# Kernel tuning notes

Measured on AMD Instinct MI355X. Metric: run time of the kernel, lower is better.

Reference implementation:

```python
import jax, jax.numpy as jnp
import numpy as np
from jax import lax

DIM = 64        # Branch(dim)
OUT = 2048      # TimesBlock out_channels == TTT model_dim
NH = 8          # num_heads
HD = OUT // NH  # 256 head dim
INNER = 4 * HD  # ttt_mlp hidden
MB = 10         # mini_batch_size
BASE_LR = 0.1   # ttt_base_lr
NK = 6          # TimesBlock num_kernels (k = 1,3,5,7,9,11)
LN_EPS = 1e-6


def _gelu(x):
    return jax.nn.gelu(x, approximate=False)


def _gelu_bwd(x):
    return 0.5 * (1.0 + lax.erf(x / jnp.sqrt(2.0))) + x * jnp.exp(-0.5 * x * x) / jnp.sqrt(2.0 * jnp.pi)


def _ttt_head(qs, ks, vs, W1h, b1h, W2h, b2h, gw, gb):
    # qs/ks/vs: [NC, MB, HD]; sequential scan over mini-batch chunks (TTT inner GD)
    eta = BASE_LR / MB

    def step(carry, chunk):
        W1c, b1c, W2c, b2c = carry
        xq, xk, xv = chunk
        Z1 = xk @ W1c + b1c              # [MB, INNER]
        A1 = _gelu(Z1)
        Z2 = A1 @ W2c + b2c              # [MB, HD]
        # grad of 0.5*||LN(Z2) - (xv - xk)||^2 wrt Z2 (fused LN l2 backward)
        tgt = xv - xk
        mu = Z2.mean(-1, keepdims=True)
        std = jnp.sqrt(Z2.var(-1, keepdims=True) + LN_EPS)
        xhat = (2 * 0 + Z2 - mu) / std
        gout = (gw * xhat + gb) - tgt
        gxh = gout * gw
        gZ2 = (gxh - gxh.mean(-1, keepdims=True) - xhat * (gxh * xhat).mean(-1, keepdims=True)) / std
        gZ1 = (gZ2 @ W2c.T) * _gelu_bwd(Z1)
        # inner-model SGD step
        W1n = W1c - eta * (xk.T @ gZ1)
        b1n = b1c - eta * gZ1.sum(0)
        W2n = W2c - eta * (A1.T @ gZ2)
        b2n = b2c - eta * gZ2.sum(0)
        # apply updated inner model to queries, post-LN + residual
        Z1q = xq @ W1n + b1n
        Z2q = _gelu(Z1q) @ W2n + b2n
        muq = Z2q.mean(-1, keepdims=True)
        stdq = jnp.sqrt(Z2q.var(-1, keepdims=True) + LN_EPS)
        out = xq + gw * ((Z2q - muq) / stdq) + gb
        return (W1n, b1n, W2n, b2n), out

    _, outs = lax.scan(step, (W1h, b1h, W2h, b2h), (qs, ks, vs))
    return outs.reshape(-1, HD)  # [T, HD]


def _forward(x, seg, conv_ws, conv_bs, wq, wk, wv, wo, W1, b1, W2, b2, ln_w, ln_b):
    B, T, C = x.shape
    xg = jnp.transpose(x, (0, 2, 1)).reshape(B, C, T // seg, seg)
    dn = ('NCHW', 'OIHW', 'NCHW')
    acc = 0.0
    for w, bc in zip(conv_ws, conv_bs):
        acc = acc + lax.conv_general_dilated(xg, w, (1, 1), 'SAME', dimension_numbers=dn) + bc[None, :, None, None]
    xb = acc / float(len(conv_ws))            # TimesBlock: mean over kernel ensemble
    xb = jax.nn.silu(xb)
    xb = jnp.transpose(xb.reshape(B, OUT, T), (0, 2, 1))  # [B, T, OUT]

    def heads(h):  # [B,T,OUT] -> [B,NH,NC,MB,HD]
        return jnp.transpose(h.reshape(B, T, NH, HD), (0, 2, 1, 3)).reshape(B, NH, T // MB, MB, HD)

    q = heads(xb @ wq.T)
    k = heads(xb @ wk.T)
    v = heads(xb @ wv.T)
    f = jax.vmap(jax.vmap(_ttt_head, in_axes=(0, 0, 0, 0, 0, 0, 0, 0, 0)),
                 in_axes=(0, 0, 0, None, None, None, None, None, None))
    o = f(q, k, v, W1, b1, W2, b2, ln_w, ln_b)  # [B, NH, T, HD]
    o = jnp.transpose(o, (0, 2, 1, 3)).reshape(B, T, OUT)
    return o @ wo.T


def setup_inputs() -> dict:
    key = jax.random.key(0)
    ks = jax.random.split(key, 24)
    B, T = 2, 400
    inp = {"x": jax.random.normal(ks[0], (B, T, DIM), jnp.float32), "seg": 20}
    for i in range(NK):
        kk = 2 * i + 1
        fan_out = OUT * kk * kk
        inp[f"conv_w{i}"] = jax.random.normal(ks[1 + i], (OUT, DIM, kk, kk), jnp.float32) * np.sqrt(2.0 / fan_out)
        inp[f"conv_b{i}"] = jnp.zeros((OUT,), jnp.float32)
    for j, nm in enumerate(["wq", "wk", "wv", "wo"]):
        inp[nm] = jax.random.normal(ks[8 + j], (OUT, OUT), jnp.float32) * 0.02
    inp["W1"] = jax.random.normal(ks[12], (NH, HD, INNER), jnp.float32) * 0.02
    inp["b1"] = jnp.zeros((NH, INNER), jnp.float32)
    inp["W2"] = jax.random.normal(ks[13], (NH, INNER, HD), jnp.float32) * 0.02
    inp["b2"] = jnp.zeros((NH, HD), jnp.float32)
    inp["ln_w"] = jnp.ones((NH, HD), jnp.float32)
    inp["ln_b"] = jnp.zeros((NH, HD), jnp.float32)
    return inp


def reference(x, seg, conv_w0, conv_b0, conv_w1, conv_b1, conv_w2, conv_b2,
              conv_w3, conv_b3, conv_w4, conv_b4, conv_w5, conv_b5,
              wq, wk, wv, wo, W1, b1, W2, b2, ln_w, ln_b):
    conv_ws = [conv_w0, conv_w1, conv_w2, conv_w3, conv_w4, conv_w5]
    conv_bs = [conv_b0, conv_b1, conv_b2, conv_b3, conv_b4, conv_b5]
    return _forward(x, seg, conv_ws, conv_bs, wq, wk, wv, wo, W1, b1, W2, b2, ln_w, ln_b)
```

## Files before the change

kernel.cpp:

```cpp
#include <hip/hip_runtime.h>


typedef __bf16 bf16x8 __attribute__((ext_vector_type(8)));
typedef float  f32x4  __attribute__((ext_vector_type(4)));

__device__ __forceinline__ unsigned short f2bf(float f){
  unsigned int u = __builtin_bit_cast(unsigned int, f);
  u += 0x7fffu + ((u >> 16) & 1u);
  return (unsigned short)(u >> 16);
}
__device__ __forceinline__ float bf2f(unsigned short b){
  unsigned int u = ((unsigned int)b) << 16;
  return __builtin_bit_cast(float, u);
}
__device__ __forceinline__ float gelu_f(float x){
  return 0.5f * x * (1.0f + erff(x * 0.70710678118654752f));
}
__device__ __forceinline__ float gelu_bwd_f(float x){
  return 0.5f * (1.0f + erff(x * 0.70710678118654752f))
       + x * __expf(-0.5f * x * x) * 0.3989422804014327f;
}

__device__ __forceinline__ float2 aload2(const float* p){
  unsigned long long v = __hip_atomic_load((const unsigned long long*)p,
                                           __ATOMIC_RELAXED, __HIP_MEMORY_SCOPE_AGENT);
  union { unsigned long long u; float2 f; } cv; cv.u = v; return cv.f;
}
__device__ __forceinline__ void aadd(float* p, float v){
  __hip_atomic_fetch_add(p, v, __ATOMIC_RELAXED, __HIP_MEMORY_SCOPE_AGENT);
}


__global__ __launch_bounds__(256) void k_weff(
    const float* __restrict__ w0, const float* __restrict__ w1,
    const float* __restrict__ w2, const float* __restrict__ w3,
    const float* __restrict__ w4, const float* __restrict__ w5,
    const float* __restrict__ b0, const float* __restrict__ b1,
    const float* __restrict__ b2, const float* __restrict__ b3,
    const float* __restrict__ b4, const float* __restrict__ b5,
    unsigned short* __restrict__ weff, float* __restrict__ bsum)
{
  extern __shared__ float sw[];
  const int off[6] = {0, 64, 640, 2240, 5376, 10560};
  const float* ws6[6] = {w0, w1, w2, w3, w4, w5};
  int o = blockIdx.x, tid = threadIdx.x;
  if (tid == 0)
    bsum[o] = b0[o] + b1[o] + b2[o] + b3[o] + b4[o] + b5[o];
#pragma unroll
  for (int i = 0; i < 6; i++){
    int kk = 2 * i + 1, sz = 64 * kk * kk;
    const float* src = ws6[i] + (size_t)o * sz;
    for (int idx = tid; idx < sz; idx += 256) sw[off[i] + idx] = src[idx];
  }
  __syncthreads();
  for (int t = tid; t < 7744; t += 256){
    int c = t / 121, dd = t % 121, di = dd / 11, dj = dd % 11;
    float s = 0.f;
#pragma unroll
    for (int i = 0; i < 6; i++){
      int kk = 2 * i + 1;
      int a = di - 5 + i, b = dj - 5 + i;
      if (a >= 0 && a < kk && b >= 0 && b < kk)
        s += sw[off[i] + (c * kk + a) * kk + b];
    }
    weff[(size_t)o * 7744 + t] = f2bf(s);
  }
}

__global__ __launch_bounds__(256) void k_im2col(
    const float* __restrict__ x, unsigned short* __restrict__ P)
{
  int idx = blockIdx.x * 256 + threadIdx.x;
  if (idx >= 800 * 7744) return;
  int n = idx / 7744, k = idx % 7744;
  int c = k / 121, dd = k % 121, di = dd / 11, dj = dd % 11;
  int b = n / 400, pos = n % 400, i = pos / 20, j = pos % 20;
  int ii = i + di - 5, jj = j + dj - 5;
  float v = 0.f;
  if (ii >= 0 && ii < 20 && jj >= 0 && jj < 20)
    v = x[((size_t)b * 400 + ii * 20 + jj) * 64 + c];
  P[idx] = f2bf(v);
}

__global__ __launch_bounds__(256) void k_wqkv(
    const float* __restrict__ wq, const float* __restrict__ wk,
    const float* __restrict__ wv, unsigned short* __restrict__ dst)
{
  int idx = blockIdx.x * 256 + threadIdx.x;
  if (idx >= 6144 * 2048) return;
  int m = idx >> 11, kk = idx & 2047;
  const float* src = (m < 2048) ? wq : ((m < 4096) ? wk : wv);
  dst[idx] = f2bf(src[(size_t)(m & 2047) * 2048 + kk]);
}

__global__ __launch_bounds__(256) void k_f2bf_copy(
    const float* __restrict__ src, unsigned short* __restrict__ dst, int n)
{
  int idx = blockIdx.x * 256 + threadIdx.x;
  if (idx < n) dst[idx] = f2bf(src[idx]);
}

__global__ __launch_bounds__(256) void k_comb_silu(
    const float* __restrict__ p0, const float* __restrict__ p1,
    const float* __restrict__ bsum, unsigned short* __restrict__ xb)
{
  int i4 = (blockIdx.x * 256 + threadIdx.x) * 4;
  float4 a = *(const float4*)&p0[i4];
  float4 b = *(const float4*)&p1[i4];
  int mm = i4 & 2047;
  float4 bs = *(const float4*)&bsum[mm];
  float v[4] = {a.x + b.x + bs.x, a.y + b.y + bs.y, a.z + b.z + bs.z, a.w + b.w + bs.w};
  ushort4 o;
#pragma unroll
  for (int i = 0; i < 4; i++){
    float t = v[i] * (1.0f / 6.0f);
    float sv = t / (1.0f + __expf(-t));
    ((unsigned short*)&o)[i] = f2bf(sv);
  }
  *(ushort4*)&xb[i4] = o;
}

__global__ __launch_bounds__(256) void k_comb_add4(
    const float* __restrict__ p, float* __restrict__ out)
{
  int i4 = (blockIdx.x * 256 + threadIdx.x) * 4;
  float4 a = *(const float4*)&p[i4];
  float4 b = *(const float4*)&p[1638400 + i4];
  float4 c = *(const float4*)&p[3276800 + i4];
  float4 d = *(const float4*)&p[4915200 + i4];
  float4 o = {a.x + b.x + c.x + d.x, a.y + b.y + c.y + d.y,
              a.z + b.z + c.z + d.z, a.w + b.w + c.w + d.w};
  *(float4*)&out[i4] = o;
}

template<int MODE>
__global__ __launch_bounds__(256, 1) void k_gemm(
    const unsigned short* __restrict__ A, const unsigned short* __restrict__ B,
    int M, int N, int lda, int ldb, int kLen,
    unsigned short* __restrict__ qb, unsigned short* __restrict__ kb,
    unsigned short* __restrict__ vb, float* __restrict__ outf)
{
  __shared__ unsigned short As[128 * 32];
  __shared__ unsigned short Bs[128 * 32];
  int tid = threadIdx.x, w = tid >> 6, l = tid & 63, qd = l >> 4, lm = l & 15;
  int m0 = blockIdx.x * 128, n0 = blockIdx.y * 128;
  int kBase = blockIdx.z * kLen;

  f32x4 acc[4][4];
#pragma unroll
  for (int i = 0; i < 4; i++)
#pragma unroll
    for (int j = 0; j < 4; j++){ acc[i][j][0]=0.f; acc[i][j][1]=0.f; acc[i][j][2]=0.f; acc[i][j][3]=0.f; }

  int nk = kLen >> 5;
  for (int kt = 0; kt < nk; kt++){
    int k0 = kBase + (kt << 5);
#pragma unroll
    for (int i = 0; i < 2; i++){
      int cidx = tid + i * 256;
      int row = cidx >> 2, kc = (cidx & 3) << 3;
      *(uint4*)&As[row * 32 + kc] = *(const uint4*)&A[(size_t)(m0 + row) * lda + k0 + kc];
      int br = n0 + row; if (br >= N) br = N - 1;
      *(uint4*)&Bs[row * 32 + kc] = *(const uint4*)&B[(size_t)br * ldb + k0 + kc];
    }
    __syncthreads();
    bf16x8 af[4], bfv[4];
#pragma unroll
    for (int i = 0; i < 4; i++)
      af[i] = *(const bf16x8*)&As[((w >> 1) * 64 + i * 16 + lm) * 32 + qd * 8];
#pragma unroll
    for (int j = 0; j < 4; j++)
      bfv[j] = *(const bf16x8*)&Bs[((w & 1) * 64 + j * 16 + lm) * 32 + qd * 8];
#pragma unroll
    for (int i = 0; i < 4; i++)
#pragma unroll
      for (int j = 0; j < 4; j++)
        acc[i][j] = __builtin_amdgcn_mfma_f32_16x16x32_bf16(af[i], bfv[j], acc[i][j], 0, 0, 0);
    __syncthreads();
  }

#pragma unroll
  for (int i = 0; i < 4; i++){
    int mBase = m0 + (w >> 1) * 64 + i * 16 + qd * 4;
#pragma unroll
    for (int j = 0; j < 4; j++){
      int n = n0 + (w & 1) * 64 + j * 16 + lm;
      if (n < N){
#pragma unroll
        for (int rr = 0; rr < 4; rr++){
          float val = acc[i][j][rr];
          int mm = mBase + rr;
          if (MODE == 1){
            int proj = mm >> 11, o = mm & 2047, hh = o >> 8, d = o & 255;
            int bh = (n / 400) * 8 + hh, tt = n % 400;
            unsigned short* dst = (proj == 0) ? qb : ((proj == 1) ? kb : vb);
            dst[((size_t)bh * 400 + tt) * 256 + d] = f2bf(val);
          } else {
            outf[(size_t)blockIdx.z * M * N + (size_t)n * M + mm] = val;
          }
        }
      }
    }
  }
}

#define O_W1BT 0
#define O_W2K  16896
#define O_W2N  33792
#define O_XKQ  52224
#define O_TGT  54864
#define O_A1   57424
#define O_A1T  58144
#define O_GZ2  60192
#define O_GZ1  62832
#define O_XQ2  64880
#define O_GZ2T 67520
#define O_XKT  73664
#define O_A1Q  79808
#define O_F32  80528
#define O_GW   81168
#define O_GB   81424
#define US_TOTAL 81680
#define TTT_LDS_BYTES (81680 * 2)

#define A1T_IDX(r, c) (O_A1T + ((((r) * 32) + (c)) ^ (((r) & 3) << 3)))
#define GZ1_IDX(r, c) (O_GZ1 + ((((r) * 32) + (c)) ^ (((r) & 3) << 3)))

#define ETA 0.01f
#define BAR_STRIDE 32

__global__ __launch_bounds__(256, 1) void k_ttt(
    const unsigned short* __restrict__ qg, const unsigned short* __restrict__ kg,
    const unsigned short* __restrict__ vg,
    const float* __restrict__ W1g, const float* __restrict__ b1g,
    const float* __restrict__ W2g, const float* __restrict__ b2g,
    const float* __restrict__ gwg, const float* __restrict__ gbg,
    float* __restrict__ z2acc, unsigned short* __restrict__ zqp,
    unsigned int* __restrict__ bar)
{
  extern __shared__ unsigned short lds[];
  float* ldsf = (float*)&lds[O_F32];

  int tid = threadIdx.x, w = tid >> 6, l = tid & 63, qd = l >> 4, lm = l & 15;
  int bid = blockIdx.x;
  int jj = bid >> 3, xx = bid & 7;
  int h  = xx + 8 * (jj >> 4);
  int sl = jj & 15;
  int hh = h & 7;

  for (int i = tid; i < US_TOTAL; i += 256) lds[i] = 0;
  __syncthreads();

  float w1r[4][4][4];
#pragma unroll
  for (int a = 0; a < 4; a++)
#pragma unroll
    for (int nt = 0; nt < 4; nt++)
#pragma unroll
      for (int rr = 0; rr < 4; rr++)
        w1r[a][nt][rr] = W1g[((size_t)hh * 256 + (4 * w + a) * 16 + qd * 4 + rr) * 1024
                             + sl * 64 + nt * 16 + lm];
  float w2r[16][4];
#pragma unroll
  for (int nt = 0; nt < 16; nt++)
#pragma unroll
    for (int rr = 0; rr < 4; rr++)
      w2r[nt][rr] = W2g[((size_t)hh * 1024 + sl * 64 + w * 16 + qd * 4 + rr) * 256
                        + nt * 16 + lm];
  if (tid < 64)  ldsf[tid] = b1g[hh * 1024 + sl * 64 + tid];
  if (tid < 256){
    ldsf[64 + tid] = b2g[hh * 256 + tid];
    lds[O_GW + tid] = f2bf(gwg[hh * 256 + tid]);
    lds[O_GB + tid] = f2bf(gbg[hh * 256 + tid]);
  }

#define WRITE_W1BF() do { \
  _Pragma("unroll") for (int a = 0; a < 4; a++){ \
    int m0i = (4 * w + a) * 16 + qd * 4; \
    _Pragma("unroll") for (int nt = 0; nt < 4; nt++){ \
      int n = nt * 16 + lm; \
      unsigned int p0 = f2bf(w1r[a][nt][0]) | ((unsigned int)f2bf(w1r[a][nt][1]) << 16); \
      unsigned int p1 = f2bf(w1r[a][nt][2]) | ((unsigned int)f2bf(w1r[a][nt][3]) << 16); \
      *(unsigned int*)&lds[O_W1BT + n * 264 + m0i]     = p0; \
      *(unsigned int*)&lds[O_W1BT + n * 264 + m0i + 2] = p1; \
    } } } while(0)

#define WRITE_W2BF() do { \
  int mB = w * 16 + qd * 4; \
  _Pragma("unroll") for (int nt = 0; nt < 16; nt++){ \
    int n = nt * 16 + lm; \
    _Pragma("unroll") for (int rr = 0; rr < 4; rr++) \
      lds[O_W2K + (mB + rr) * 264 + n] = f2bf(w2r[nt][rr]); \
    unsigned int p0 = f2bf(w2r[nt][0]) | ((unsigned int)f2bf(w2r[nt][1]) << 16); \
    unsigned int p1 = f2bf(w2r[nt][2]) | ((unsigned int)f2bf(w2r[nt][3]) << 16); \
    *(unsigned int*)&lds[O_W2N + n * 72 + mB]     = p0; \
    *(unsigned int*)&lds[O_W2N + n * 72 + mB + 2] = p1; \
  } } while(0)

  const size_t hb2 = (size_t)h * 400 * 256;

  unsigned int kreg[5], vreg[5];

#define LOAD_XK_REGS(NCH) do { \
  const unsigned int* kp = (const unsigned int*)(kg + hb2 + (size_t)(NCH) * 2560); \
  const unsigned int* vp = (const unsigned int*)(vg + hb2 + (size_t)(NCH) * 2560); \
  _Pragma("unroll") for (int i5 = 0; i5 < 5; i5++){ \
    kreg[i5] = kp[i5 * 256 + tid]; \
    vreg[i5] = vp[i5 * 256 + tid]; \
  } } while(0)

#define COMMIT_XK_TGT() do { \
  _Pragma("unroll") for (int i5 = 0; i5 < 5; i5++){ \
    int f2i = i5 * 256 + tid; \
    unsigned int ku = kreg[i5], vu = vreg[i5]; \
    int row = f2i >> 7, col = (f2i & 127) * 2; \
    *(unsigned int*)&lds[O_XKQ + row * 264 + col] = ku; \
    lds[O_XKT + col * 24 + row]       = (unsigned short)(ku & 0xffffu); \
    lds[O_XKT + (col + 1) * 24 + row] = (unsigned short)(ku >> 16); \
    float kv0 = bf2f((unsigned short)(ku & 0xffffu)), kv1 = bf2f((unsigned short)(ku >> 16)); \
    float vv0 = bf2f((unsigned short)(vu & 0xffffu)), vv1 = bf2f((unsigned short)(vu >> 16)); \
    unsigned int tu = (unsigned int)f2bf(vv0 - kv0) | ((unsigned int)f2bf(vv1 - kv1) << 16); \
    *(unsigned int*)&lds[O_TGT + row * 256 + col] = tu; \
  } } while(0)

#define LOAD_XQ(NCH) do { \
  const unsigned int* qp = (const unsigned int*)(qg + hb2 + (size_t)(NCH) * 2560); \
  _Pragma("unroll") for (int i5 = 0; i5 < 5; i5++){ \
    int f2i = i5 * 256 + tid; \
    unsigned int qu = qp[f2i]; \
    int row = f2i >> 7, col = (f2i & 127) * 2; \
    *(unsigned int*)&lds[O_XQ2 + row * 264 + col] = qu; \
  } } while(0)

  WRITE_W1BF();
  WRITE_W2BF();
  LOAD_XK_REGS(0);
  COMMIT_XK_TGT();
  LOAD_XQ(0);
  __syncthreads();

  for (int nch = 0; nch < 40; nch++){
    const size_t chunkBase = (size_t)(h * 40 + nch) * 10 * 256;

    bf16x8 w1f[8];
#pragma unroll
    for (int ks = 0; ks < 8; ks++)
      w1f[ks] = *(const bf16x8*)&lds[O_W1BT + (w * 16 + lm) * 264 + ks * 32 + qd * 8];
    float b1n = ldsf[w * 16 + lm];

    f32x4 z1a; z1a[0]=0.f; z1a[1]=0.f; z1a[2]=0.f; z1a[3]=0.f;
#pragma unroll
    for (int ks = 0; ks < 8; ks++){
      bf16x8 av = *(const bf16x8*)&lds[O_XKQ + lm * 264 + ks * 32 + qd * 8];
      z1a = __builtin_amdgcn_mfma_f32_16x16x32_bf16(av, w1f[ks], z1a, 0, 0, 0);
    }
    float z1v[4];
#pragma unroll
    for (int rr = 0; rr < 4; rr++){
      z1v[rr] = z1a[rr] + b1n;
      int mr = qd * 4 + rr;
      if (mr < 10){
        float a1 = gelu_f(z1v[rr]);
        unsigned short ab = f2bf(a1);
        lds[O_A1 + mr * 72 + w * 16 + lm] = ab;
        lds[A1T_IDX(w * 16 + lm, mr)] = ab;
      }
    }
    __syncthreads();

    bf16x8 a1f[2], w2f[4][2];
#pragma unroll
    for (int ks = 0; ks < 2; ks++)
      a1f[ks] = *(const bf16x8*)&lds[O_A1 + lm * 72 + ks * 32 + qd * 8];
#pragma unroll
    for (int nt4 = 0; nt4 < 4; nt4++)
#pragma unroll
      for (int ks = 0; ks < 2; ks++)
        w2f[nt4][ks] = *(const bf16x8*)&lds[O_W2N + ((4 * w + nt4) * 16 + lm) * 72 + ks * 32 + qd * 8];

#pragma unroll
    for (int nt4 = 0; nt4 < 4; nt4++){
      int nt = 4 * w + nt4;
      f32x4 p; p[0]=0.f; p[1]=0.f; p[2]=0.f; p[3]=0.f;
#pragma unroll
      for (int ks = 0; ks < 2; ks++)
        p = __builtin_amdgcn_mfma_f32_16x16x32_bf16(a1f[ks], w2f[nt4][ks], p, 0, 0, 0);
#pragma unroll
      for (int rr = 0; rr < 4; rr++){
        int mr = qd * 4 + rr;
        if (mr < 10)
          aadd(&z2acc[chunkBase + (size_t)mr * 256 + nt * 16 + lm], p[rr]);
      }
    }
    __syncthreads();

    if (tid == 0)
      __hip_atomic_fetch_add(bar + h * BAR_STRIDE, 1u, __ATOMIC_RELAXED, __HIP_MEMORY_SCOPE_AGENT);

    if (nch + 1 < 40)
      LOAD_XK_REGS(nch + 1);

    if (nch > 0){
      f32x4 zq; zq[0]=0.f; zq[1]=0.f; zq[2]=0.f; zq[3]=0.f;
#pragma unroll
      for (int ks = 0; ks < 8; ks++){
        bf16x8 av = *(const bf16x8*)&lds[O_XQ2 + lm * 264 + ks * 32 + qd * 8];
        zq = __builtin_amdgcn_mfma_f32_16x16x32_bf16(av, w1f[ks], zq, 0, 0, 0);
      }
#pragma unroll
      for (int rr = 0; rr < 4; rr++){
        int mr = qd * 4 + rr;
        if (mr < 10)
          lds[O_A1Q + mr * 72 + w * 16 + lm] = f2bf(gelu_f(zq[rr] + b1n));
      }
    }
    __syncthreads();

    if (nch > 0){
      LOAD_XQ(nch);
      unsigned short* zq_out = zqp + ((size_t)(h * 16 + sl) * 40 + (nch - 1)) * 2560;
      bf16x8 a1qf[2];
#pragma unroll
      for (int ks = 0; ks < 2; ks++)
        a1qf[ks] = *(const bf16x8*)&lds[O_A1Q + lm * 72 + ks * 32 + qd * 8];
#pragma unroll
      for (int nt4 = 0; nt4 < 4; nt4++){
        int nt = 4 * w + nt4;
        f32x4 p; p[0]=0.f; p[1]=0.f; p[2]=0.f; p[3]=0.f;
#pragma unroll
        for (int ks = 0; ks < 2; ks++)
          p = __builtin_amdgcn_mfma_f32_16x16x32_bf16(a1qf[ks], w2f[nt4][ks], p, 0, 0, 0);
        float bb = (sl == 0) ? ldsf[64 + nt * 16 + lm] : 0.f;
#pragma unroll
        for (int rr = 0; rr < 4; rr++){
          int mr = qd * 4 + rr;
          if (mr < 10)
            zq_out[mr * 256 + nt * 16 + lm] = f2bf(p[rr] + bb);
        }
      }
    }

    if (tid == 0){
      unsigned int target = 16u * (unsigned int)(nch + 1);
      unsigned int spins = 0;
      while (__hip_atomic_load(bar + h * BAR_STRIDE, __ATOMIC_RELAXED, __HIP_MEMORY_SCOPE_AGENT) < target
             && spins < 8000000u){ spins++; __builtin_amdgcn_s_sleep(1); }
    }
    __syncthreads();

    for (int r2 = w; r2 < 10; r2 += 4){
      int c0 = l * 4;
      const float* bp = &z2acc[chunkBase + (size_t)r2 * 256 + c0];
      float2 u01 = aload2(bp);
      float2 u23 = aload2(bp + 2);
      float zz[4] = {u01.x, u01.y, u23.x, u23.y};
      float s1 = 0.f, s2 = 0.f;
#pragma unroll
      for (int i = 0; i < 4; i++){ zz[i] += ldsf[64 + c0 + i]; s1 += zz[i]; s2 += zz[i] * zz[i]; }
#pragma unroll
      for (int off = 32; off >= 1; off >>= 1){ s1 += __shfl_xor(s1, off, 64); s2 += __shfl_xor(s2, off, 64); }
      float mu = s1 * (1.f / 256.f);
      float var = s2 * (1.f / 256.f) - mu * mu;
      float rstd = rsqrtf(var + 1e-6f);
      float xh[4], gx[4];
      float t1 = 0.f, t2 = 0.f;
#pragma unroll
      for (int i = 0; i < 4; i++){
        xh[i] = (zz[i] - mu) * rstd;
        float gwv = bf2f(lds[O_GW + c0 + i]), gbv = bf2f(lds[O_GB + c0 + i]);
        float tg = bf2f(lds[O_TGT + r2 * 256 + c0 + i]);
        float go = gwv * xh[i] + gbv - tg;
        gx[i] = go * gwv;
        t1 += gx[i]; t2 += gx[i] * xh[i];
      }
#pragma unroll
      for (int off = 32; off >= 1; off >>= 1){ t1 += __shfl_xor(t1, off, 64); t2 += __shfl_xor(t2, off, 64); }
      float m1 = t1 * (1.f / 256.f), m2 = t2 * (1.f / 256.f);
      float g0 = (gx[0] - m1 - xh[0] * m2) * rstd;
      float g1 = (gx[1] - m1 - xh[1] * m2) * rstd;
      float g2 = (gx[2] - m1 - xh[2] * m2) * rstd;
      float g3 = (gx[3] - m1 - xh[3] * m2) * rstd;
      unsigned int p0 = f2bf(g0) | ((unsigned int)f2bf(g1) << 16);
      unsigned int p1 = f2bf(g2) | ((unsigned int)f2bf(g3) << 16);
      *(unsigned int*)&lds[O_GZ2 + r2 * 264 + c0]     = p0;
      *(unsigned int*)&lds[O_GZ2 + r2 * 264 + c0 + 2] = p1;
    }
    __syncthreads();

    {
      float sum = 0.f;
#pragma unroll
      for (int r2 = 0; r2 < 10; r2++){
        unsigned short g = lds[O_GZ2 + r2 * 264 + tid];
        lds[O_GZ2T + tid * 24 + r2] = g;
        sum += bf2f(g);
      }
      ldsf[64 + tid] -= ETA * sum;
    }
    {
      f32x4 g1a; g1a[0]=0.f; g1a[1]=0.f; g1a[2]=0.f; g1a[3]=0.f;
#pragma unroll
      for (int ks = 0; ks < 8; ks++){
        bf16x8 av = *(const bf16x8*)&lds[O_GZ2 + lm * 264 + ks * 32 + qd * 8];
        bf16x8 bv = *(const bf16x8*)&lds[O_W2K + (w * 16 + lm) * 264 + ks * 32 + qd * 8];
        g1a = __builtin_amdgcn_mfma_f32_16x16x32_bf16(av, bv, g1a, 0, 0, 0);
      }
#pragma unroll
      for (int rr = 0; rr < 4; rr++){
        int mr = qd * 4 + rr;
        if (mr < 10){
          float gz1 = g1a[rr] * gelu_bwd_f(z1v[rr]);
          lds[GZ1_IDX(w * 16 + lm, mr)] = f2bf(gz1);
        }
      }
    }
    __syncthreads();

    if (tid < 64){
      float sum = 0.f;
#pragma unroll
      for (int kx = 0; kx < 10; kx++) sum += bf2f(lds[GZ1_IDX(tid, kx)]);
      ldsf[tid] -= ETA * sum;
    }
#pragma unroll
    for (int a = 0; a < 4; a++){
      int mt = 4 * w + a;
      bf16x8 av = *(const bf16x8*)&lds[O_XKT + (mt * 16 + lm) * 24 + (qd & 1) * 8];
#pragma unroll
      for (int nt = 0; nt < 4; nt++){
        bf16x8 bv = *(const bf16x8*)&lds[GZ1_IDX(nt * 16 + lm, qd * 8)];
        f32x4 d; d[0]=0.f; d[1]=0.f; d[2]=0.f; d[3]=0.f;
        d = __builtin_amdgcn_mfma_f32_16x16x32_bf16(av, bv, d, 0, 0, 0);
#pragma unroll
        for (int rr = 0; rr < 4; rr++) w1r[a][nt][rr] -= ETA * d[rr];
      }
    }
    {
      bf16x8 av2 = *(const bf16x8*)&lds[A1T_IDX(w * 16 + lm, qd * 8)];
#pragma unroll
      for (int nt = 0; nt < 16; nt++){
        bf16x8 bv = *(const bf16x8*)&lds[O_GZ2T + (nt * 16 + lm) * 24 + (qd & 1) * 8];
        f32x4 d; d[0]=0.f; d[1]=0.f; d[2]=0.f; d[3]=0.f;
        d = __builtin_amdgcn_mfma_f32_16x16x32_bf16(av2, bv, d, 0, 0, 0);
#pragma unroll
        for (int rr = 0; rr < 4; rr++) w2r[nt][rr] -= ETA * d[rr];
      }
    }
    WRITE_W1BF();
    WRITE_W2BF();
    __syncthreads();

    if (nch + 1 < 40){
      COMMIT_XK_TGT();
    }
    __syncthreads();
  }

  {
    f32x4 zq; zq[0]=0.f; zq[1]=0.f; zq[2]=0.f; zq[3]=0.f;
#pragma unroll
    for (int ks = 0; ks < 8; ks++){
      bf16x8 av = *(const bf16x8*)&lds[O_XQ2 + lm * 264 + ks * 32 + qd * 8];
      bf16x8 bv = *(const bf16x8*)&lds[O_W1BT + (w * 16 + lm) * 264 + ks * 32 + qd * 8];
      zq = __builtin_amdgcn_mfma_f32_16x16x32_bf16(av, bv, zq, 0, 0, 0);
    }
    float b1n = ldsf[w * 16 + lm];
#pragma unroll
    for (int rr = 0; rr < 4; rr++){
      int mr = qd * 4 + rr;
      if (mr < 10)
        lds[O_A1Q + mr * 72 + w * 16 + lm] = f2bf(gelu_f(zq[rr] + b1n));
    }
  }
  __syncthreads();
  {
    unsigned short* zq_out = zqp + ((size_t)(h * 16 + sl) * 40 + 39) * 2560;
#pragma unroll
    for (int nt4 = 0; nt4 < 4; nt4++){
      int nt = 4 * w + nt4;
      f32x4 p; p[0]=0.f; p[1]=0.f; p[2]=0.f; p[3]=0.f;
#pragma unroll
      for (int ks = 0; ks < 2; ks++){
        bf16x8 av = *(const bf16x8*)&lds[O_A1Q + lm * 72 + ks * 32 + qd * 8];
        bf16x8 bv = *(const bf16x8*)&lds[O_W2N + (nt * 16 + lm) * 72 + ks * 32 + qd * 8];
        p = __builtin_amdgcn_mfma_f32_16x16x32_bf16(av, bv, p, 0, 0, 0);
      }
      float bb = (sl == 0) ? ldsf[64 + nt * 16 + lm] : 0.f;
#pragma unroll
      for (int rr = 0; rr < 4; rr++){
        int mr = qd * 4 + rr;
        if (mr < 10)
          zq_out[mr * 256 + nt * 16 + lm] = f2bf(p[rr] + bb);
      }
    }
  }
}

__global__ __launch_bounds__(256) void k_lnout(
    const unsigned short* __restrict__ zqp, const unsigned short* __restrict__ qg,
    const float* __restrict__ gwg, const float* __restrict__ gbg,
    unsigned short* __restrict__ obf)
{
  int w = threadIdx.x >> 6, l = threadIdx.x & 63;
  int gr = blockIdx.x * 4 + w;
  int h = gr / 400, t = gr % 400, hh = h & 7, b = h >> 3;
  int nch = t / 10, mr = t % 10;
  int c0 = l * 4;
  float z[4] = {0.f, 0.f, 0.f, 0.f};
#pragma unroll
  for (int sl = 0; sl < 16; sl++){
    const unsigned short* zp = zqp + (((size_t)(h * 16 + sl) * 40 + nch) * 10 + mr) * 256 + c0;
    ushort4 u = *(const ushort4*)zp;
    z[0] += bf2f(u.x); z[1] += bf2f(u.y); z[2] += bf2f(u.z); z[3] += bf2f(u.w);
  }
  float s1 = 0.f, s2 = 0.f;
#pragma unroll
  for (int i = 0; i < 4; i++){ s1 += z[i]; s2 += z[i] * z[i]; }
#pragma unroll
  for (int off = 32; off >= 1; off >>= 1){ s1 += __shfl_xor(s1, off, 64); s2 += __shfl_xor(s2, off, 64); }
  float mu = s1 * (1.f / 256.f);
  float var = s2 * (1.f / 256.f) - mu * mu;
  float rstd = rsqrtf(var + 1e-6f);
  const unsigned short* qp = &qg[((size_t)h * 400 + t) * 256];
  ushort4 qu = *(const ushort4*)&qp[c0];
  float qv[4] = {bf2f(qu.x), bf2f(qu.y), bf2f(qu.z), bf2f(qu.w)};
  unsigned short* op = &obf[((size_t)(b * 400 + t)) * 2048 + hh * 256];
#pragma unroll
  for (int i = 0; i < 4; i++){
    float xh = (z[i] - mu) * rstd;
    float o = qv[i] + gwg[hh * 256 + c0 + i] * xh + gbg[hh * 256 + c0 + i];
    op[c0 + i] = f2bf(o);
  }
}

#define WS_WEFF   0u
#define WS_P      31719424u
#define WS_WQKV   44109824u
#define WS_WOB    52428800u
#define WS_Z2ACC  62722048u
#define WS_XB     69275648u
#define WS_Q      72552448u
#define WS_K      75829248u
#define WS_V      79106048u
#define WS_OBF    82382848u
#define WS_BSUM   85659648u
#define WS_BAR    85667840u

extern "C" void kernel_launch(void* const* d_in, const int* in_sizes, int n_in,
                              void* d_out, int out_size, void* d_ws, size_t ws_size,
                              hipStream_t stream)
{
  (void)in_sizes; (void)n_in; (void)out_size; (void)ws_size;
  const float* x  = (const float*)d_in[0];
  const float* cw[6]; const float* cb[6];
  for (int i = 0; i < 6; i++){ cw[i] = (const float*)d_in[2 + 2 * i]; cb[i] = (const float*)d_in[3 + 2 * i]; }
  const float* wq  = (const float*)d_in[14];
  const float* wk  = (const float*)d_in[15];
  const float* wv  = (const float*)d_in[16];
  const float* wo  = (const float*)d_in[17];
  const float* W1  = (const float*)d_in[18];
  const float* b1  = (const float*)d_in[19];
  const float* W2  = (const float*)d_in[20];
  const float* b2  = (const float*)d_in[21];
  const float* lnw = (const float*)d_in[22];
  const float* lnb = (const float*)d_in[23];
  float* outf = (float*)d_out;

  char* wsb = (char*)d_ws;
  unsigned short* weff = (unsigned short*)(wsb + WS_WEFF);
  unsigned short* P    = (unsigned short*)(wsb + WS_P);
  unsigned short* wqkv = (unsigned short*)(wsb + WS_WQKV);
  unsigned short* wob  = (unsigned short*)(wsb + WS_WOB);
  unsigned short* xb   = (unsigned short*)(wsb + WS_XB);
  unsigned short* qb   = (unsigned short*)(wsb + WS_Q);
  unsigned short* kb   = (unsigned short*)(wsb + WS_K);
  unsigned short* vb   = (unsigned short*)(wsb + WS_V);
  float* z2acc = (float*)(wsb + WS_Z2ACC);
  unsigned short* zqp = (unsigned short*)(wsb + WS_WEFF);
  unsigned short* obf = (unsigned short*)(wsb + WS_OBF);
  float* bsum = (float*)(wsb + WS_BSUM);
  unsigned int* bar = (unsigned int*)(wsb + WS_BAR);
  float* g0part = (float*)(wsb + WS_Q);
  float* g2part = (float*)(wsb + WS_WEFF);

  hipMemsetAsync(bar, 0, 16 * BAR_STRIDE * 4, stream);
  hipFuncSetAttribute(reinterpret_cast<const void*>(k_ttt),
                      hipFuncAttributeMaxDynamicSharedMemorySize, TTT_LDS_BYTES);
  hipFuncSetAttribute(reinterpret_cast<const void*>(k_weff),
                      hipFuncAttributeMaxDynamicSharedMemorySize, 18304 * 4);

  k_weff<<<2048, 256, 18304 * 4, stream>>>(cw[0], cw[1], cw[2], cw[3], cw[4], cw[5],
                                           cb[0], cb[1], cb[2], cb[3], cb[4], cb[5],
                                           weff, bsum);
  k_im2col<<<(800 * 7744 + 255) / 256, 256, 0, stream>>>(x, P);
  k_wqkv<<<(6144 * 2048 + 255) / 256, 256, 0, stream>>>(wq, wk, wv, wqkv);

  k_gemm<2><<<dim3(16, 7, 2), 256, 0, stream>>>(weff, P, 2048, 800, 7744, 7744, 3872,
                                                nullptr, nullptr, nullptr, g0part);
  k_comb_silu<<<1600, 256, 0, stream>>>(g0part, g0part + 1638400, bsum, xb);

  k_gemm<1><<<dim3(48, 7, 1), 256, 0, stream>>>(wqkv, xb, 6144, 800, 2048, 2048, 2048,
                                                qb, kb, vb, nullptr);

  k_f2bf_copy<<<(2048 * 2048 + 255) / 256, 256, 0, stream>>>(wo, wob, 2048 * 2048);
  hipMemsetAsync(z2acc, 0, 16 * 40 * 10 * 256 * 4, stream);

  k_ttt<<<256, 256, TTT_LDS_BYTES, stream>>>(qb, kb, vb, W1, b1, W2, b2, lnw, lnb,
                                             z2acc, zqp, bar);
  k_lnout<<<1600, 256, 0, stream>>>(zqp, qb, lnw, lnb, obf);

  k_gemm<2><<<dim3(16, 7, 4), 256, 0, stream>>>(wob, obf, 2048, 800, 2048, 2048, 512,
                                                nullptr, nullptr, nullptr, g2part);
  k_comb_add4<<<1600, 256, 0, stream>>>(g2part, outf);
}
```

Before: 1.033 ms.

## Vectorize weight casts, use direct global-to-LDS loads in GEMM, batch TTT loads

After: 1.049 ms. About the same (+1.5%).

```diff
diff --git a/kernel.cpp b/kernel.cpp
--- a/kernel.cpp
+++ b/kernel.cpp
@@ -82,22 +82,27 @@
   P[idx] = f2bf(v);
 }
 
-__global__ __launch_bounds__(256) void k_wqkv(
+__global__ __launch_bounds__(256) void k_wprep(
     const float* __restrict__ wq, const float* __restrict__ wk,
     const float* __restrict__ wv, unsigned short* __restrict__ dst)
 {
-  int idx = blockIdx.x * 256 + threadIdx.x;
-  if (idx >= 6144 * 2048) return;
-  int m = idx >> 11, kk = idx & 2047;
+  int i4 = (blockIdx.x * 256 + threadIdx.x) * 4;
+  int m = i4 >> 11, kk = i4 & 2047;
   const float* src = (m < 2048) ? wq : ((m < 4096) ? wk : wv);
-  dst[idx] = f2bf(src[(size_t)(m & 2047) * 2048 + kk]);
-}
-
-__global__ __launch_bounds__(256) void k_f2bf_copy(
-    const float* __restrict__ src, unsigned short* __restrict__ dst, int n)
-{
-  int idx = blockIdx.x * 256 + threadIdx.x;
-  if (idx < n) dst[idx] = f2bf(src[idx]);
+  float4 v = *(const float4*)&src[(size_t)(m & 2047) * 2048 + kk];
+  ushort4 o;
+  o.x = f2bf(v.x); o.y = f2bf(v.y); o.z = f2bf(v.z); o.w = f2bf(v.w);
+  *(ushort4*)&dst[i4] = o;
+}
+
+__global__ __launch_bounds__(256) void k_wocopy(
+    const float* __restrict__ wo, unsigned short* __restrict__ wob)
+{
+  int i4 = (blockIdx.x * 256 + threadIdx.x) * 4;
+  float4 v = *(const float4*)&wo[i4];
+  ushort4 o;
+  o.x = f2bf(v.x); o.y = f2bf(v.y); o.z = f2bf(v.z); o.w = f2bf(v.w);
+  *(ushort4*)&wob[i4] = o;
 }
 
 __global__ __launch_bounds__(256) void k_comb_silu(
@@ -152,16 +157,24 @@
 #pragma unroll
     for (int j = 0; j < 4; j++){ acc[i][j][0]=0.f; acc[i][j][1]=0.f; acc[i][j][2]=0.f; acc[i][j][3]=0.f; }
 
+  int c2a = w * 2;
+  int rA = l >> 2;
+  int kc = (l & 3) << 3;
+
   int nk = kLen >> 5;
   for (int kt = 0; kt < nk; kt++){
     int k0 = kBase + (kt << 5);
 #pragma unroll
     for (int i = 0; i < 2; i++){
-      int cidx = tid + i * 256;
-      int row = cidx >> 2, kc = (cidx & 3) << 3;
-      *(uint4*)&As[row * 32 + kc] = *(const uint4*)&A[(size_t)(m0 + row) * lda + k0 + kc];
+      int c2 = c2a + i;
+      int row = c2 * 16 + rA;
+      __builtin_amdgcn_global_load_lds(
+          (const __attribute__((address_space(1))) void*)&A[(size_t)(m0 + row) * lda + k0 + kc],
+          (__attribute__((address_space(3))) void*)&As[c2 * 512], 16, 0, 0);
       int br = n0 + row; if (br >= N) br = N - 1;
-      *(uint4*)&Bs[row * 32 + kc] = *(const uint4*)&B[(size_t)br * ldb + k0 + kc];
+      __builtin_amdgcn_global_load_lds(
+          (const __attribute__((address_space(1))) void*)&B[(size_t)br * ldb + k0 + kc],
+          (__attribute__((address_space(3))) void*)&Bs[c2 * 512], 16, 0, 0);
     }
     __syncthreads();
     bf16x8 af[4], bfv[4];
@@ -448,42 +461,59 @@
     }
     __syncthreads();
 
-    for (int r2 = w; r2 < 10; r2 += 4){
-      int c0 = l * 4;
-      const float* bp = &z2acc[chunkBase + (size_t)r2 * 256 + c0];
-      float2 u01 = aload2(bp);
-      float2 u23 = aload2(bp + 2);
-      float zz[4] = {u01.x, u01.y, u23.x, u23.y};
-      float s1 = 0.f, s2 = 0.f;
-#pragma unroll
-      for (int i = 0; i < 4; i++){ zz[i] += ldsf[64 + c0 + i]; s1 += zz[i]; s2 += zz[i] * zz[i]; }
-#pragma unroll
-      for (int off = 32; off >= 1; off >>= 1){ s1 += __shfl_xor(s1, off, 64); s2 += __shfl_xor(s2, off, 64); }
-      float mu = s1 * (1.f / 256.f);
-      float var = s2 * (1.f / 256.f) - mu * mu;
-      float rstd = rsqrtf(var + 1e-6f);
-      float xh[4], gx[4];
-      float t1 = 0.f, t2 = 0.f;
-#pragma unroll
-      for (int i = 0; i < 4; i++){
-        xh[i] = (zz[i] - mu) * rstd;
-        float gwv = bf2f(lds[O_GW + c0 + i]), gbv = bf2f(lds[O_GB + c0 + i]);
-        float tg = bf2f(lds[O_TGT + r2 * 256 + c0 + i]);
-        float go = gwv * xh[i] + gbv - tg;
-        gx[i] = go * gwv;
-        t1 += gx[i]; t2 += gx[i] * xh[i];
-      }
-#pragma unroll
-      for (int off = 32; off >= 1; off >>= 1){ t1 += __shfl_xor(t1, off, 64); t2 += __shfl_xor(t2, off, 64); }
-      float m1 = t1 * (1.f / 256.f), m2 = t2 * (1.f / 256.f);
-      float g0 = (gx[0] - m1 - xh[0] * m2) * rstd;
-      float g1 = (gx[1] - m1 - xh[1] * m2) * rstd;
-      float g2 = (gx[2] - m1 - xh[2] * m2) * rstd;
-      float g3 = (gx[3] - m1 - xh[3] * m2) * rstd;
-      unsigned int p0 = f2bf(g0) | ((unsigned int)f2bf(g1) << 16);
-      unsigned int p1 = f2bf(g2) | ((unsigned int)f2bf(g3) << 16);
-      *(unsigned int*)&lds[O_GZ2 + r2 * 264 + c0]     = p0;
-      *(unsigned int*)&lds[O_GZ2 + r2 * 264 + c0 + 2] = p1;
+    {
+      float zr[3][4];
+#pragma unroll
+      for (int q2 = 0; q2 < 3; q2++){
+        int r2 = w + q2 * 4;
+        if (r2 < 10){
+          const float* bp = &z2acc[chunkBase + (size_t)r2 * 256 + l * 4];
+          float2 u01 = aload2(bp);
+          float2 u23 = aload2(bp + 2);
+          zr[q2][0] = u01.x; zr[q2][1] = u01.y; zr[q2][2] = u23.x; zr[q2][3] = u23.y;
+        }
+      }
+#pragma unroll
+      for (int q2 = 0; q2 < 3; q2++){
+        int r2 = w + q2 * 4;
+        if (r2 < 10){
+          int c0 = l * 4;
+          float zz[4];
+          float s1 = 0.f, s2 = 0.f;
+#pragma unroll
+          for (int i = 0; i < 4; i++){
+            zz[i] = zr[q2][i] + ldsf[64 + c0 + i];
+            s1 += zz[i]; s2 += zz[i] * zz[i];
+          }
+#pragma unroll
+          for (int off = 32; off >= 1; off >>= 1){ s1 += __shfl_xor(s1, off, 64); s2 += __shfl_xor(s2, off, 64); }
+          float mu = s1 * (1.f / 256.f);
+          float var = s2 * (1.f / 256.f) - mu * mu;
+          float rstd = rsqrtf(var + 1e-6f);
+          float xh[4], gx[4];
+          float t1 = 0.f, t2 = 0.f;
+#pragma unroll
+          for (int i = 0; i < 4; i++){
+            xh[i] = (zz[i] - mu) * rstd;
+            float gwv = bf2f(lds[O_GW + c0 + i]), gbv = bf2f(lds[O_GB + c0 + i]);
+            float tg = bf2f(lds[O_TGT + r2 * 256 + c0 + i]);
+            float go = gwv * xh[i] + gbv - tg;
+            gx[i] = go * gwv;
+            t1 += gx[i]; t2 += gx[i] * xh[i];
+          }
+#pragma unroll
+          for (int off = 32; off >= 1; off >>= 1){ t1 += __shfl_xor(t1, off, 64); t2 += __shfl_xor(t2, off, 64); }
+          float m1 = t1 * (1.f / 256.f), m2 = t2 * (1.f / 256.f);
+          float g0 = (gx[0] - m1 - xh[0] * m2) * rstd;
+          float g1 = (gx[1] - m1 - xh[1] * m2) * rstd;
+          float g2 = (gx[2] - m1 - xh[2] * m2) * rstd;
+          float g3 = (gx[3] - m1 - xh[3] * m2) * rstd;
+          unsigned int p0 = f2bf(g0) | ((unsigned int)f2bf(g1) << 16);
+          unsigned int p1 = f2bf(g2) | ((unsigned int)f2bf(g3) << 16);
+          *(unsigned int*)&lds[O_GZ2 + r2 * 264 + c0]     = p0;
+          *(unsigned int*)&lds[O_GZ2 + r2 * 264 + c0 + 2] = p1;
+        }
+      }
     }
     __syncthreads();
 
@@ -693,7 +723,7 @@
                                            cb[0], cb[1], cb[2], cb[3], cb[4], cb[5],
                                            weff, bsum);
   k_im2col<<<(800 * 7744 + 255) / 256, 256, 0, stream>>>(x, P);
-  k_wqkv<<<(6144 * 2048 + 255) / 256, 256, 0, stream>>>(wq, wk, wv, wqkv);
+  k_wprep<<<12288, 256, 0, stream>>>(wq, wk, wv, wqkv);
 
   k_gemm<2><<<dim3(16, 7, 2), 256, 0, stream>>>(weff, P, 2048, 800, 7744, 7744, 3872,
                                                 nullptr, nullptr, nullptr, g0part);
@@ -702,7 +732,7 @@
   k_gemm<1><<<dim3(48, 7, 1), 256, 0, stream>>>(wqkv, xb, 6144, 800, 2048, 2048, 2048,
                                                 qb, kb, vb, nullptr);
 
-  k_f2bf_copy<<<(2048 * 2048 + 255) / 256, 256, 0, stream>>>(wo, wob, 2048 * 2048);
+  k_wocopy<<<4096, 256, 0, stream>>>(wo, wob);
   hipMemsetAsync(z2acc, 0, 16 * 40 * 10 * 256 * 4, stream);
 
   k_ttt<<<256, 256, TTT_LDS_BYTES, stream>>>(qb, kb, vb, W1, b1, W2, b2, lnw, lnb,
```
